# Kernel tuning notes

Hardware: AMD Instinct MI355X
Metric: run time of the kernel (lower is better)

The kernel has to match this reference:

```python
import jax, jax.numpy as jnp
import numpy as np

N_NODES = 10000
N_CHANNELS = 32
DIM = 3
N_LAYERS = 2
BASIS_R = 2   # basis_rank_max
FEAT_R = 2    # feature_rank_max
NU_MAX = 3
N_EDGES = 160000


def setup_inputs() -> dict:
    key = jax.random.key(0)
    ks = jax.random.split(key, 8)
    pos = jax.random.normal(ks[0], (N_NODES, DIM), jnp.float32)
    edge_index = jax.random.randint(ks[1], (2, N_EDGES), 0, N_NODES, dtype=jnp.int32)
    atoms = jnp.zeros((N_NODES,), jnp.int32)  # Embedding(1, C) -> all indices 0
    emb_w = jax.random.normal(ks[2], (1, N_CHANNELS), jnp.float32)
    W_ab = 0.1 * jax.random.normal(ks[3], (N_LAYERS, BASIS_R + 1, FEAT_R + 1, N_CHANNELS, N_CHANNELS), jnp.float32)
    ws_w = 0.1 * jax.random.normal(ks[4], (N_LAYERS, FEAT_R + 1, NU_MAX, N_CHANNELS), jnp.float32)
    channel_w = 0.1 * jax.random.normal(ks[5], (N_LAYERS, FEAT_R + 1, N_NODES, N_CHANNELS, N_CHANNELS), jnp.float32)
    message_w = 0.1 * jax.random.normal(ks[6], (N_LAYERS, FEAT_R + 1, N_NODES, N_CHANNELS, N_CHANNELS), jnp.float32)
    return dict(pos=pos, edge_index=edge_index, atoms=atoms, emb_w=emb_w,
                W_ab=W_ab, ws_w=ws_w, channel_w=channel_w, message_w=message_w)


def _u_powers(u, max_rank):
    # u: (E, DIM) unit vectors; returns [u^{\otimes k}] flattened to (E, DIM**k)
    pows = [jnp.ones((u.shape[0], 1), u.dtype)]
    for _ in range(max_rank):
        pows.append((pows[-1][:, :, None] * u[:, None, :]).reshape(u.shape[0], -1))
    return pows


def reference(pos, edge_index, atoms, emb_w, W_ab, ws_w, channel_w, message_w):
    src, dst = edge_index[0], edge_index[1]
    rel = pos[dst] - pos[src]                                   # (E, 3)
    u = rel / (jnp.linalg.norm(rel, axis=-1, keepdims=True) + 1e-9)
    u_pow = _u_powers(u, max(BASIS_R, FEAT_R))

    # node features h[c]: (N, C, 3**c) (trailing Cartesian indices flattened)
    h = [jnp.zeros((N_NODES, N_CHANNELS, DIM ** c), pos.dtype) for c in range(FEAT_R + 1)]
    h[0] = h[0] + emb_w[atoms][:, :, None]

    for l in range(N_LAYERS):
        # ---- atomic basis: A_c(i) = sum_{j->i} sum_a W^{(c,a)} (h_a(j) . u^{ox a}) u^{ox c}
        A = []
        for c in range(BASIS_R + 1):
            acc = jnp.zeros((N_EDGES, N_CHANNELS), pos.dtype)
            for a in range(FEAT_R + 1):
                s = jnp.einsum('ecd,ed->ec', h[a][src], u_pow[a])   # full contraction -> scalar
                acc = acc + jnp.einsum('jk,ek->ej', W_ab[l, c, a], s)
            contrib = acc[:, :, None] * u_pow[c][:, None, :]        # (E, C, 3**c)
            A.append(jax.ops.segment_sum(contrib, dst, num_segments=N_NODES))
        # ---- weighted sum (product basis): m_c = sum_nu w_{c,nu} (A_0)^{nu-1} A_c
        s0 = A[0][..., 0]                                           # (N, C)
        messages = []
        for c in range(FEAT_R + 1):
            m = jnp.zeros_like(A[c])
            p = jnp.ones_like(s0)
            for nu in range(NU_MAX):
                m = m + ws_w[l, c, nu][None, :, None] * (p[:, :, None] * A[c])
                p = p * s0
            messages.append(m)
        # ---- update (MACE eq. 11): per-node channel mixing of old state + messages
        h = [jnp.einsum('ijk,ikd->ijd', channel_w[l, c], h[c])
             + jnp.einsum('ijk,ikd->ijd', message_w[l, c], messages[c])
             for c in range(FEAT_R + 1)]

    # concatenate ranks along flattened Cartesian axis: (N, C, 1+3+9)
    return jnp.concatenate(h, axis=-1)
```

## Files before the change

kernel.cpp:

```cpp
#include <hip/hip_runtime.h>

#define N_NODES 10000
#define N_CH    32
#define N_EDGES 160000
#define HPAD    16
#define SLOTS   8

__device__ __forceinline__ float dot4(float4 a, float4 b) {
    return a.x*b.x + a.y*b.y + a.z*b.z + a.w*b.w;
}

__global__ void k_hist(const int* __restrict__ ei, int* __restrict__ deg) {
    int e = blockIdx.x * 256 + threadIdx.x;
    atomicAdd(&deg[ei[N_EDGES + e]], 1);
}

__global__ __launch_bounds__(1024) void k_scan(const int* __restrict__ deg,
                                               int* __restrict__ offs,
                                               int* __restrict__ cursor) {
    __shared__ int part[1024];
    const int t = threadIdx.x;
    const int base = t * 10;
    int s = 0;
#pragma unroll
    for (int r = 0; r < 10; ++r) { int i = base + r; if (i < N_NODES) s += deg[i]; }
    part[t] = s;
    __syncthreads();
    for (int off = 1; off < 1024; off <<= 1) {
        int v = (t >= off) ? part[t - off] : 0;
        __syncthreads();
        part[t] += v;
        __syncthreads();
    }
    int run = (t > 0) ? part[t - 1] : 0;
#pragma unroll
    for (int r = 0; r < 10; ++r) {
        int i = base + r;
        if (i < N_NODES) { offs[i] = run; cursor[i] = run; run += deg[i]; }
    }
    if (t == 0) offs[N_NODES] = N_EDGES;
}

__global__ void k_scatter(const int* __restrict__ ei, const float* __restrict__ pos,
                          int* __restrict__ cursor, int* __restrict__ ssrc,
                          float4* __restrict__ us4) {
    int e = blockIdx.x * 256 + threadIdx.x;
    int s = ei[e], d = ei[N_EDGES + e];
    float rx = pos[d*3+0] - pos[s*3+0];
    float ry = pos[d*3+1] - pos[s*3+1];
    float rz = pos[d*3+2] - pos[s*3+2];
    float inv = 1.0f / (sqrtf(rx*rx + ry*ry + rz*rz) + 1e-9f);
    int p = atomicAdd(&cursor[d], 1);
    ssrc[p] = s;
    us4[p] = make_float4(rx*inv, ry*inv, rz*inv, 0.f);
}

template<int LAYER>
__global__ __launch_bounds__(256, 2) void k_gather(
    const float* __restrict__ hPrev,
    const float* __restrict__ emb_w,
    const int* __restrict__ ssrc,
    const float4* __restrict__ us4,
    const int* __restrict__ offs,
    const float* __restrict__ W_ab,
    const float* __restrict__ ws_w,
    float* __restrict__ msg)
{
    constexpr int AMAX = (LAYER == 0) ? 1 : 3;
    __shared__ __align__(16) float Tlds[SLOTS * AMAX * 10 * 32];

    const int slot = threadIdx.x >> 5;
    const int j    = threadIdx.x & 31;
    const int node = blockIdx.x * SLOTS + slot;

    const int e0 = offs[node], e1 = offs[node + 1];

    if (LAYER == 0) {
        float U[10];
#pragma unroll
        for (int d = 0; d < 10; ++d) U[d] = 0.f;
        for (int idx = e0; idx < e1; ++idx) {
            const float4 u = us4[idx];
            U[0] += 1.f;
            U[1] += u.x;      U[2] += u.y;      U[3] += u.z;
            U[4] += u.x*u.x;  U[5] += u.x*u.y;  U[6] += u.x*u.z;
            U[7] += u.y*u.y;  U[8] += u.y*u.z;  U[9] += u.z*u.z;
        }
        const float s0 = emb_w[j];
#pragma unroll
        for (int d = 0; d < 10; ++d)
            Tlds[(slot * 10 + d) * 32 + j] = s0 * U[d];
    } else {
        float T0[10], T1[10], T2[10];
#pragma unroll
        for (int d = 0; d < 10; ++d) { T0[d] = 0.f; T1[d] = 0.f; T2[d] = 0.f; }
        for (int idx = e0; idx < e1; ++idx) {
            const int src = ssrc[idx];
            const float4 u = us4[idx];
            const float* hr = hPrev + ((size_t)(src * N_CH + j)) * HPAD;
            const float4 a0 = *(const float4*)(hr);
            const float4 a1 = *(const float4*)(hr + 4);
            const float4 a2 = *(const float4*)(hr + 8);
            const float h12 = hr[12];

            const float xx = u.x*u.x, xy = u.x*u.y, xz = u.x*u.z;
            const float yy = u.y*u.y, yz = u.y*u.z, zz = u.z*u.z;

            const float s0 = a0.x;
            const float s1 = a0.y*u.x + a0.z*u.y + a0.w*u.z;
            const float s2 = a1.x*xx + (a1.y + a1.w)*xy + (a1.z + a2.z)*xz
                           + a2.x*yy + (a2.y + a2.w)*yz + h12*zz;

            T0[0] += s0;       T1[0] += s1;       T2[0] += s2;
            T0[1] += s0*u.x;   T1[1] += s1*u.x;   T2[1] += s2*u.x;
            T0[2] += s0*u.y;   T1[2] += s1*u.y;   T2[2] += s2*u.y;
            T0[3] += s0*u.z;   T1[3] += s1*u.z;   T2[3] += s2*u.z;
            T0[4] += s0*xx;    T1[4] += s1*xx;    T2[4] += s2*xx;
            T0[5] += s0*xy;    T1[5] += s1*xy;    T2[5] += s2*xy;
            T0[6] += s0*xz;    T1[6] += s1*xz;    T2[6] += s2*xz;
            T0[7] += s0*yy;    T1[7] += s1*yy;    T2[7] += s2*yy;
            T0[8] += s0*yz;    T1[8] += s1*yz;    T2[8] += s2*yz;
            T0[9] += s0*zz;    T1[9] += s1*zz;    T2[9] += s2*zz;
        }
#pragma unroll
        for (int d = 0; d < 10; ++d) {
            Tlds[((slot * 3 + 0) * 10 + d) * 32 + j] = T0[d];
            Tlds[((slot * 3 + 1) * 10 + d) * 32 + j] = T1[d];
            Tlds[((slot * 3 + 2) * 10 + d) * 32 + j] = T2[d];
        }
    }

    __syncthreads();

    float acc[10];
#pragma unroll
    for (int d = 0; d < 10; ++d) acc[d] = 0.f;

#pragma unroll
    for (int c = 0; c < 3; ++c) {
        const int dlo = (c == 0) ? 0 : ((c == 1) ? 1 : 4);
        const int dhi = (c == 0) ? 1 : ((c == 1) ? 4 : 10);
#pragma unroll
        for (int a = 0; a < AMAX; ++a) {
            const float* wrow = W_ab + (((size_t)((LAYER * 3 + c) * 3 + a)) << 10) + (j << 5);
#pragma unroll
            for (int k4 = 0; k4 < 8; ++k4) {
                const float4 w4 = *(const float4*)(wrow + k4 * 4);
                for (int d = dlo; d < dhi; ++d) {
                    const float4 t4 = *(const float4*)&Tlds[((slot * AMAX + a) * 10 + d) * 32 + k4 * 4];
                    acc[d] += dot4(w4, t4);
                }
            }
        }
    }

    const float s0n = acc[0];
    const float s0sq = s0n * s0n;
    float poly[3];
#pragma unroll
    for (int c = 0; c < 3; ++c) {
        const float* wsp = ws_w + ((size_t)((LAYER * 3 + c) * 3)) * 32 + j;
        poly[c] = wsp[0] + wsp[32] * s0n + wsp[64] * s0sq;
    }
    {
        const int mExp[13] = {0, 1, 2, 3, 4, 5, 6, 5, 7, 8, 6, 8, 9};
#pragma unroll
        for (int m = 0; m < 13; ++m) {
            const float p = (m == 0) ? poly[0] : ((m < 4) ? poly[1] : poly[2]);
            msg[((size_t)node * 13 + m) * 32 + j] = p * acc[mExp[m]];
        }
    }
}

template<int LAYER>
__global__ __launch_bounds__(256, 4) void k_update(
    const float* __restrict__ hPrev,
    const float* __restrict__ emb_w,
    const float* __restrict__ msg,
    const float* __restrict__ cw,
    const float* __restrict__ mw,
    float* __restrict__ hOut)
{
    constexpr int MSZ = SLOTS * 13 * 32;
    constexpr int HSZ = (LAYER == 0) ? 32 : MSZ;
    __shared__ __align__(16) float hls[HSZ];
    __shared__ __align__(16) float mls[MSZ];

    const int slot = threadIdx.x >> 5;
    const int j    = threadIdx.x & 31;
    const int node = blockIdx.x * SLOTS + slot;

#pragma unroll
    for (int m = 0; m < 13; ++m)
        mls[(slot * 13 + m) * 32 + j] = msg[((size_t)node * 13 + m) * 32 + j];

    if (LAYER == 0) {
        if (threadIdx.x < 32) hls[threadIdx.x] = emb_w[threadIdx.x];
    } else {
        const float* hr = hPrev + ((size_t)(node * N_CH + j)) * HPAD;
        const float4 a0 = *(const float4*)(hr);
        const float4 a1 = *(const float4*)(hr + 4);
        const float4 a2 = *(const float4*)(hr + 8);
        const float h12 = hr[12];
        const float hv[13] = {a0.x, a0.y, a0.z, a0.w, a1.x, a1.y, a1.z, a1.w,
                              a2.x, a2.y, a2.z, a2.w, h12};
#pragma unroll
        for (int m = 0; m < 13; ++m) hls[(slot * 13 + m) * 32 + j] = hv[m];
    }
    __syncthreads();

    float out[13];
#pragma unroll
    for (int m = 0; m < 13; ++m) out[m] = 0.f;

#pragma unroll
    for (int c = 0; c < 3; ++c) {
        const int mlo = (c == 0) ? 0 : ((c == 1) ? 1 : 4);
        const int mhi = (c == 0) ? 1 : ((c == 1) ? 4 : 13);
        const size_t wb = (((size_t)(LAYER * 3 + c) * N_NODES + node) * 32 + j) * 32;
        const float4* mwr = (const float4*)(mw + wb);
        if (LAYER == 0) {
            if (c == 0) {
                const float4* cwr = (const float4*)(cw + wb);
#pragma unroll
                for (int k4 = 0; k4 < 8; ++k4) {
                    const float4 c4 = cwr[k4];
                    const float4 m4 = mwr[k4];
                    out[0] += dot4(c4, *(const float4*)&hls[k4 * 4])
                            + dot4(m4, *(const float4*)&mls[(slot * 13) * 32 + k4 * 4]);
                }
            } else {
#pragma unroll
                for (int k4 = 0; k4 < 8; ++k4) {
                    const float4 m4 = mwr[k4];
                    for (int m = mlo; m < mhi; ++m)
                        out[m] += dot4(m4, *(const float4*)&mls[(slot * 13 + m) * 32 + k4 * 4]);
                }
            }
        } else {
            const float4* cwr = (const float4*)(cw + wb);
#pragma unroll
            for (int k4 = 0; k4 < 8; ++k4) {
                const float4 c4 = cwr[k4];
                const float4 m4 = mwr[k4];
                for (int m = mlo; m < mhi; ++m) {
                    out[m] += dot4(c4, *(const float4*)&hls[(slot * 13 + m) * 32 + k4 * 4])
                            + dot4(m4, *(const float4*)&mls[(slot * 13 + m) * 32 + k4 * 4]);
                }
            }
        }
    }

    if (LAYER == 0) {
        float* orow = hOut + ((size_t)(node * N_CH + j)) * HPAD;
        *(float4*)(orow)     = make_float4(out[0], out[1], out[2],  out[3]);
        *(float4*)(orow + 4) = make_float4(out[4], out[5], out[6],  out[7]);
        *(float4*)(orow + 8) = make_float4(out[8], out[9], out[10], out[11]);
        orow[12] = out[12];
    } else {
        float* ols = mls;
#pragma unroll
        for (int m = 0; m < 13; ++m)
            ols[slot * 416 + j * 13 + m] = out[m];
        __syncthreads();
        float4* ob4 = (float4*)(hOut + (size_t)blockIdx.x * (SLOTS * N_CH * 13));
        const float4* ls4 = (const float4*)ols;
        for (int i = threadIdx.x; i < (SLOTS * N_CH * 13) / 4; i += 256)
            ob4[i] = ls4[i];
    }
}

extern "C" void kernel_launch(void* const* d_in, const int* in_sizes, int n_in,
                              void* d_out, int out_size, void* d_ws, size_t ws_size,
                              hipStream_t stream) {
    const float* pos   = (const float*)d_in[0];
    const int*   ei    = (const int*)d_in[1];
    const float* emb_w = (const float*)d_in[3];
    const float* W_ab  = (const float*)d_in[4];
    const float* ws_w  = (const float*)d_in[5];
    const float* cw    = (const float*)d_in[6];
    const float* mw    = (const float*)d_in[7];
    float* out = (float*)d_out;

    char* ws = (char*)d_ws;
    float* hB   = (float*)ws;  ws += (size_t)N_NODES * N_CH * HPAD * 4;
    float* msgB = (float*)ws;  ws += (size_t)N_NODES * 13 * N_CH * 4;
    float4* us4 = (float4*)ws; ws += (size_t)N_EDGES * 16;
    int* ssrc   = (int*)ws;    ws += (size_t)N_EDGES * 4;
    int* offs   = (int*)ws;    ws += (size_t)(N_NODES + 16) * 4;
    int* cursor = (int*)ws;    ws += (size_t)N_NODES * 4;
    int* deg    = (int*)ws;    ws += (size_t)N_NODES * 4;

    hipMemsetAsync(deg, 0, N_NODES * 4, stream);
    k_hist<<<N_EDGES / 256, 256, 0, stream>>>(ei, deg);
    k_scan<<<1, 1024, 0, stream>>>(deg, offs, cursor);
    k_scatter<<<N_EDGES / 256, 256, 0, stream>>>(ei, pos, cursor, ssrc, us4);

    k_gather<0><<<N_NODES / SLOTS, 256, 0, stream>>>(nullptr, emb_w, ssrc, us4, offs,
                                                     W_ab, ws_w, msgB);
    k_update<0><<<N_NODES / SLOTS, 256, 0, stream>>>(nullptr, emb_w, msgB, cw, mw, hB);
    k_gather<1><<<N_NODES / SLOTS, 256, 0, stream>>>(hB, emb_w, ssrc, us4, offs,
                                                     W_ab, ws_w, msgB);
    k_update<1><<<N_NODES / SLOTS, 256, 0, stream>>>(hB, emb_w, msgB, cw, mw, out);
}
```

Baseline: 763.4 us.

## Coalesce per-node weight loads in update kernel via lane-split rows and shuffle reduction

The update kernel used to have each lane read one full 32-float weight row, which made neighbouring lanes touch addresses 128 bytes apart. Now each group of 8 lanes shares a row, so a wavefront reads contiguous 512-byte chunks of the weight slab with float4 loads. Partial dot products are summed across the 8 lanes with xor shuffles and written to a new shared-memory output tile. This aims to cut uncoalesced global traffic on the large channel and message weights. The cost is extra shuffles, more shared memory per block (which may lower occupancy), and an added barrier.

Result: faster. 698.9 us (-8.4%).

```diff
diff --git a/kernel.cpp b/kernel.cpp
--- a/kernel.cpp
+++ b/kernel.cpp
@@ -183,21 +183,25 @@
 {
     constexpr int MSZ = SLOTS * 13 * 32;
     constexpr int HSZ = (LAYER == 0) ? 32 : MSZ;
+    constexpr int OSZ = SLOTS * 32 * 13;
     __shared__ __align__(16) float hls[HSZ];
     __shared__ __align__(16) float mls[MSZ];
+    __shared__ __align__(16) float ols[OSZ];
 
     const int slot = threadIdx.x >> 5;
-    const int j    = threadIdx.x & 31;
+    const int l    = threadIdx.x & 31;
     const int node = blockIdx.x * SLOTS + slot;
+    const int g    = l >> 3;
+    const int cl   = l & 7;
 
 #pragma unroll
     for (int m = 0; m < 13; ++m)
-        mls[(slot * 13 + m) * 32 + j] = msg[((size_t)node * 13 + m) * 32 + j];
+        mls[(slot * 13 + m) * 32 + l] = msg[((size_t)node * 13 + m) * 32 + l];
 
     if (LAYER == 0) {
         if (threadIdx.x < 32) hls[threadIdx.x] = emb_w[threadIdx.x];
     } else {
-        const float* hr = hPrev + ((size_t)(node * N_CH + j)) * HPAD;
+        const float* hr = hPrev + ((size_t)(node * N_CH + l)) * HPAD;
         const float4 a0 = *(const float4*)(hr);
         const float4 a1 = *(const float4*)(hr + 4);
         const float4 a2 = *(const float4*)(hr + 8);
@@ -205,64 +209,53 @@
         const float hv[13] = {a0.x, a0.y, a0.z, a0.w, a1.x, a1.y, a1.z, a1.w,
                               a2.x, a2.y, a2.z, a2.w, h12};
 #pragma unroll
-        for (int m = 0; m < 13; ++m) hls[(slot * 13 + m) * 32 + j] = hv[m];
-    }
-    __syncthreads();
-
-    float out[13];
-#pragma unroll
-    for (int m = 0; m < 13; ++m) out[m] = 0.f;
+        for (int m = 0; m < 13; ++m) hls[(slot * 13 + m) * 32 + l] = hv[m];
+    }
+    __syncthreads();
 
 #pragma unroll
     for (int c = 0; c < 3; ++c) {
         const int mlo = (c == 0) ? 0 : ((c == 1) ? 1 : 4);
         const int mhi = (c == 0) ? 1 : ((c == 1) ? 4 : 13);
-        const size_t wb = (((size_t)(LAYER * 3 + c) * N_NODES + node) * 32 + j) * 32;
-        const float4* mwr = (const float4*)(mw + wb);
-        if (LAYER == 0) {
-            if (c == 0) {
-                const float4* cwr = (const float4*)(cw + wb);
-#pragma unroll
-                for (int k4 = 0; k4 < 8; ++k4) {
-                    const float4 c4 = cwr[k4];
-                    const float4 m4 = mwr[k4];
-                    out[0] += dot4(c4, *(const float4*)&hls[k4 * 4])
-                            + dot4(m4, *(const float4*)&mls[(slot * 13) * 32 + k4 * 4]);
+        const bool useC = (LAYER == 1) || (c == 0);
+        const size_t slabBase = ((size_t)(LAYER * 3 + c) * N_NODES + node) * 1024;
+        const float* cwS = cw + slabBase;
+        const float* mwS = mw + slabBase;
+#pragma unroll
+        for (int q = 0; q < 8; ++q) {
+            const int off = q * 128 + l * 4;
+            const float4 m4 = *(const float4*)(mwS + off);
+            float4 c4 = make_float4(0.f, 0.f, 0.f, 0.f);
+            if (useC) c4 = *(const float4*)(cwS + off);
+            const int row = 4 * q + g;
+            for (int m = mlo; m < mhi; ++m) {
+                const float4 v4 = *(const float4*)&mls[(slot * 13 + m) * 32 + cl * 4];
+                float p = dot4(m4, v4);
+                if (useC) {
+                    const float4 h4 = (LAYER == 0)
+                        ? *(const float4*)&hls[cl * 4]
+                        : *(const float4*)&hls[(slot * 13 + m) * 32 + cl * 4];
+                    p += dot4(c4, h4);
                 }
-            } else {
-#pragma unroll
-                for (int k4 = 0; k4 < 8; ++k4) {
-                    const float4 m4 = mwr[k4];
-                    for (int m = mlo; m < mhi; ++m)
-                        out[m] += dot4(m4, *(const float4*)&mls[(slot * 13 + m) * 32 + k4 * 4]);
-                }
+                p += __shfl_xor(p, 1);
+                p += __shfl_xor(p, 2);
+                p += __shfl_xor(p, 4);
+                if (cl == 0) ols[(slot * 32 + row) * 13 + m] = p;
             }
-        } else {
-            const float4* cwr = (const float4*)(cw + wb);
-#pragma unroll
-            for (int k4 = 0; k4 < 8; ++k4) {
-                const float4 c4 = cwr[k4];
-                const float4 m4 = mwr[k4];
-                for (int m = mlo; m < mhi; ++m) {
-                    out[m] += dot4(c4, *(const float4*)&hls[(slot * 13 + m) * 32 + k4 * 4])
-                            + dot4(m4, *(const float4*)&mls[(slot * 13 + m) * 32 + k4 * 4]);
-                }
-            }
-        }
-    }
+        }
+    }
+    __syncthreads();
 
     if (LAYER == 0) {
-        float* orow = hOut + ((size_t)(node * N_CH + j)) * HPAD;
-        *(float4*)(orow)     = make_float4(out[0], out[1], out[2],  out[3]);
-        *(float4*)(orow + 4) = make_float4(out[4], out[5], out[6],  out[7]);
-        *(float4*)(orow + 8) = make_float4(out[8], out[9], out[10], out[11]);
-        orow[12] = out[12];
+        float o[13];
+#pragma unroll
+        for (int m = 0; m < 13; ++m) o[m] = ols[(slot * 32 + l) * 13 + m];
+        float* orow = hOut + ((size_t)(node * N_CH + l)) * HPAD;
+        *(float4*)(orow)     = make_float4(o[0], o[1], o[2],  o[3]);
+        *(float4*)(orow + 4) = make_float4(o[4], o[5], o[6],  o[7]);
+        *(float4*)(orow + 8) = make_float4(o[8], o[9], o[10], o[11]);
+        orow[12] = o[12];
     } else {
-        float* ols = mls;
-#pragma unroll
-        for (int m = 0; m < 13; ++m)
-            ols[slot * 416 + j * 13 + m] = out[m];
-        __syncthreads();
         float4* ob4 = (float4*)(hOut + (size_t)blockIdx.x * (SLOTS * N_CH * 13));
         const float4* ls4 = (const float4*)ols;
         for (int i = threadIdx.x; i < (SLOTS * N_CH * 13) / 4; i += 256)
```
